# Performance work log

Measured on AMD Instinct MI355X. Metric: run time of the kernel, lower is better.

The kernel has to match this reference:

```python
import jax, jax.numpy as jnp
import numpy as np
from jax import lax

DIM = 256
NH = 16          # num_heads; head_dim = DIM//NH == NH (required by scale broadcast)
HD = DIM // NH   # 16
HID = int(DIM * 1.0)  # mlp hidden (ffn_expansion_factor=1.0)
B, H, W = 4, 128, 128
EPS = 1e-5


def _conv(x, w, pad, groups=1):
    # x: NCHW, w: OIHW
    return lax.conv_general_dilated(x, w, (1, 1), [(pad, pad), (pad, pad)],
                                    dimension_numbers=('NCHW', 'OIHW', 'NCHW'),
                                    feature_group_count=groups)


def _ln(x, w, b):
    # WithBias LayerNorm over channel axis (torch does it in b,(hw),c layout -> axis=c)
    mu = x.mean(1, keepdims=True)
    var = ((x - mu) ** 2).mean(1, keepdims=True)
    return (x - mu) / jnp.sqrt(var + EPS) * w[None, :, None, None] + b[None, :, None, None]


def setup_inputs() -> dict:
    key = jax.random.key(0)
    ks = jax.random.split(key, 12)
    s = 0.02
    return {
        'x': jax.random.normal(ks[0], (B, DIM, H, W), jnp.float32),
        'ln1_w': jnp.ones((DIM,), jnp.float32),
        'ln1_b': jnp.zeros((DIM,), jnp.float32),
        'conv3_w': jax.random.normal(ks[1], (DIM, 1, 3, 3), jnp.float32) * s,
        'conv3_b': jnp.zeros((DIM,), jnp.float32),
        'conv5_w': jax.random.normal(ks[2], (DIM, 1, 5, 5), jnp.float32) * s,
        'conv5_b': jnp.zeros((DIM,), jnp.float32),
        'qkv_w': jax.random.normal(ks[3], (3 * DIM, DIM), jnp.float32) * s,  # 1x1 conv, no bias
        'scale': jnp.ones((NH, 1, 1), jnp.float32),
        'g1_w': jax.random.normal(ks[4], (DIM // 4, DIM), jnp.float32) * s,
        'g1_b': jnp.zeros((DIM // 4,), jnp.float32),
        'g2_w': jax.random.normal(ks[5], (2, DIM // 4), jnp.float32) * s,
        'g2_b': jnp.zeros((2,), jnp.float32),
        'proj_w': jax.random.normal(ks[6], (DIM, DIM), jnp.float32) * s,
        'proj_b': jnp.zeros((DIM,), jnp.float32),
        'ln2_w': jnp.ones((DIM,), jnp.float32),
        'ln2_b': jnp.zeros((DIM,), jnp.float32),
        'pin_w': jax.random.normal(ks[7], (2 * HID, DIM), jnp.float32) * s,  # 1x1, bias=False
        'dw_w': jax.random.normal(ks[8], (2 * HID, 2, 3, 3), jnp.float32) * s,  # groups=HID
        'pout_w': jax.random.normal(ks[9], (DIM, HID), jnp.float32) * s,
    }


def _forward(x, ln1_w, ln1_b, conv3_w, conv3_b, conv5_w, conv5_b, qkv_w, scale,
             g1_w, g1_b, g2_w, g2_b, proj_w, proj_b, ln2_w, ln2_b, pin_w, dw_w, pout_w):
    b, c, h, w = x.shape
    # ---- token mixer (CAFormer) ----
    y = _ln(x, ln1_w, ln1_b)
    conv_feat = (_conv(y, conv3_w, 1, groups=DIM) + conv3_b[None, :, None, None]
                 + _conv(y, conv5_w, 2, groups=DIM) + conv5_b[None, :, None, None])
    qkv = jnp.einsum('oc,bchw->bohw', qkv_w, y)  # (b, 3c, h, w)
    q, k, v = jnp.split(qkv.reshape(b, 3, NH, HD, h * w), 3, axis=1)
    q, k, v = q[:, 0], k[:, 0], v[:, 0]  # (b, nh, hd, h*w)
    # L2 normalize over entire flattened spatial extent (F.normalize, eps=1e-12)
    q = q / jnp.maximum(jnp.linalg.norm(q, axis=-1, keepdims=True), 1e-12)
    k = k / jnp.maximum(jnp.linalg.norm(k, axis=-1, keepdims=True), 1e-12)
    q4 = q.reshape(b, NH, HD, h, w)
    k4 = k.reshape(b, NH, HD, h, w)
    v4 = v.reshape(b, NH, HD, h, w)
    # scale (nh,1,1) right-aligned against (b,nh,hd,x,x): broadcasts along hd axis
    sc = scale.reshape(1, 1, NH, 1, 1)
    # horizontal (row) attention: per (b,head,hd-channel), rows attend to rows
    attn_h = jax.nn.softmax(jnp.einsum('bhdxy,bhdzy->bhdxz', q4, k4) * sc, axis=-1)
    out_h = jnp.einsum('bhdxz,bhdzy->bhdxy', attn_h, v4).reshape(b, c, h, w)
    # vertical (column) attention
    qt, kt, vt = (t.swapaxes(-1, -2) for t in (q4, k4, v4))  # (b,nh,hd,w,h)
    attn_v = jax.nn.softmax(jnp.einsum('bhdyx,bhdzx->bhdyz', qt, kt) * sc, axis=-1)
    out_v = jnp.einsum('bhdyz,bhdzx->bhdyx', attn_v, vt).swapaxes(-1, -2).reshape(b, c, h, w)
    attn_feat = out_h + out_v
    # gate: GAP -> 1x1 -> relu -> 1x1 -> softmax over the 2 branch logits
    gp = y.mean((2, 3))  # (b, c)
    g = jax.nn.relu(gp @ g1_w.T + g1_b)
    g = jax.nn.softmax(g @ g2_w.T + g2_b, axis=-1)  # (b, 2)
    cw = g[:, 0][:, None, None, None]
    aw = g[:, 1][:, None, None, None]
    mixed = cw * conv_feat + aw * attn_feat
    tm = jnp.einsum('oc,bchw->bohw', proj_w, mixed) + proj_b[None, :, None, None]
    x = x + tm
    # ---- MLP ----
    y2 = _ln(x, ln2_w, ln2_b)
    p = jnp.einsum('oc,bchw->bohw', pin_w, y2)  # (b, 2*HID, h, w)
    dwo = _conv(p, dw_w, 1, groups=HID)         # grouped 3x3, 2 ch per group
    x1, x2 = dwo[:, :HID], dwo[:, HID:]
    m = jax.nn.gelu(x1, approximate=False) * x2
    mlp = jnp.einsum('oc,bchw->bohw', pout_w, m)
    return x + mlp


def reference(x, ln1_w, ln1_b, conv3_w, conv3_b, conv5_w, conv5_b, qkv_w, scale,
              g1_w, g1_b, g2_w, g2_b, proj_w, proj_b, ln2_w, ln2_b, pin_w, dw_w, pout_w):
    return _forward(x, ln1_w, ln1_b, conv3_w, conv3_b, conv5_w, conv5_b, qkv_w, scale,
                    g1_w, g1_b, g2_w, g2_b, proj_w, proj_b, ln2_w, ln2_b, pin_w, dw_w, pout_w)
```

## Files before the change

### kernel.cpp

```cpp
#include <hip/hip_runtime.h>
#include <hip/hip_bf16.h>
#include <math.h>

#define DIMC 256
#define NB   4
#define HH   128
#define WW   128
#define HWs  16384
#define HID  256
#define C2   512
#define EPSf 1e-5f

typedef __hip_bfloat16 bf;
typedef unsigned short u16;
typedef unsigned int   u32;
typedef float f32x4  __attribute__((ext_vector_type(4)));
typedef u32   u32x4  __attribute__((ext_vector_type(4)));
typedef short bf16x8 __attribute__((ext_vector_type(8)));

__device__ __forceinline__ float b2f(bf v){ return __bfloat162float(v); }
__device__ __forceinline__ bf    f2b(float v){ return __float2bfloat16(v); }
__device__ __forceinline__ float ldf(const float* p){ return *p; }
__device__ __forceinline__ float ldf(const bf* p){ return __bfloat162float(*p); }
__device__ __forceinline__ void  sto(float* p, float v){ *p = v; }
__device__ __forceinline__ void  sto(bf* p, float v){ *p = f2b(v); }
__device__ __forceinline__ void unpack2(u32 u, float& a, float& b){
  union{u32 x; float f;} lo, hi;
  lo.x = u << 16; hi.x = u & 0xffff0000u;
  a = lo.f; b = hi.f;
}
__device__ __forceinline__ u32 pack2(float a, float b){
  bf h0 = f2b(a), h1 = f2b(b);
  return (u32)*(u16*)&h0 | ((u32)*(u16*)&h1 << 16);
}
__device__ __forceinline__ void unp4(uint2 u, float* d){
  unpack2(u.x, d[0], d[1]); unpack2(u.y, d[2], d[3]);
}

__device__ __forceinline__ float gelu_exact(float v){
  return 0.5f*v*(1.0f + erff(v*0.70710678118654752f));
}

__global__ __launch_bounds__(256) void cvt_kernel(const float* __restrict__ s,
    u16* __restrict__ d, int n){
  int i = blockIdx.x*256 + threadIdx.x;
  if (i < n){ bf h = f2b(s[i]); d[i] = *(u16*)&h; }
}

template<typename TI>
__global__ __launch_bounds__(256) void ln_kernel(const TI* __restrict__ x,
    const float* __restrict__ w, const float* __restrict__ bb, bf* __restrict__ y){
  int p = blockIdx.x*256 + threadIdx.x;
  int b  = p >> 14;
  int sp = p & (HWs-1);
  const TI* xb = x + (size_t)b*DIMC*HWs + sp;
  float s = 0.f, s2 = 0.f;
  for(int c=0;c<DIMC;c++){ float v = ldf(xb + (size_t)c*HWs); s += v; s2 += v*v; }
  float mu   = s * (1.0f/DIMC);
  float var  = s2 * (1.0f/DIMC) - mu*mu;
  float rinv = rsqrtf(var + EPSf);
  bf* yb = y + (size_t)b*DIMC*HWs + sp;
  for(int c=0;c<DIMC;c++){
    float v = ldf(xb + (size_t)c*HWs);
    yb[(size_t)c*HWs] = f2b((v - mu)*rinv*w[c] + bb[c]);
  }
}

__global__ __launch_bounds__(256) void gp_kernel(const bf* __restrict__ y, float* __restrict__ gp){
  int bc = blockIdx.x;
  const bf* pl = y + (size_t)bc*HWs;
  float s = 0.f;
  for(int i=threadIdx.x;i<HWs;i+=256) s += b2f(pl[i]);
  __shared__ float red[256];
  red[threadIdx.x] = s; __syncthreads();
  for(int o=128;o>0;o>>=1){
    if(threadIdx.x<o) red[threadIdx.x] += red[threadIdx.x+o];
    __syncthreads();
  }
  if(threadIdx.x==0) gp[bc] = red[0]*(1.0f/HWs);
}

__global__ __launch_bounds__(256) void gate_kernel(const float* __restrict__ gp,
    const float* __restrict__ g1w, const float* __restrict__ g1b,
    const float* __restrict__ g2w, const float* __restrict__ g2b,
    float* __restrict__ cwaw){
  __shared__ float h[NB][64];
  __shared__ float zz[NB][2];
  int t = threadIdx.x;
  int b = t >> 6, j = t & 63;
  const float* gpb = gp + b*DIMC;
  const float* wr  = g1w + j*DIMC;
  float s = g1b[j];
  for(int c=0;c<DIMC;c++) s += gpb[c]*wr[c];
  h[b][j] = fmaxf(s, 0.f);
  __syncthreads();
  if (t < 8){
    int b2 = t >> 1, o = t & 1;
    float z = g2b[o];
    const float* w2 = g2w + o*64;
    for(int q=0;q<64;q++) z += w2[q]*h[b2][q];
    zz[b2][o] = z;
  }
  __syncthreads();
  if (t < 4){
    float z0 = zz[t][0], z1 = zz[t][1];
    float mm = fmaxf(z0,z1);
    float e0 = __expf(z0-mm), e1 = __expf(z1-mm);
    float inv = 1.0f/(e0+e1);
    cwaw[2*t]   = e0*inv;
    cwaw[2*t+1] = e1*inv;
  }
}

__global__ __launch_bounds__(256) void dwconv_kernel(const bf* __restrict__ y,
    const float* __restrict__ w3, const float* __restrict__ b3,
    const float* __restrict__ w5, const float* __restrict__ b5,
    bf* __restrict__ out){
  int bi = blockIdx.x;
  int strip = bi & 7;
  int c  = (bi >> 3) & 255;
  int b  = bi >> 11;
  int t = threadIdx.x;
  int sx = t & 15, ry = t >> 4;
  int hy = strip*16 + ry;
  int x0 = sx << 3;
  const u16* pl = (const u16*)y + ((size_t)(b*DIMC + c))*HWs;

  float kc[25];
  #pragma unroll
  for(int i=0;i<25;i++) kc[i] = w5[c*25+i];
  #pragma unroll
  for(int di=0;di<3;di++)
    #pragma unroll
    for(int dj=0;dj<3;dj++)
      kc[(di+1)*5 + (dj+1)] += w3[c*9 + di*3 + dj];
  float bia = b3[c] + b5[c];

  float acc[8];
  #pragma unroll
  for(int j=0;j<8;j++) acc[j] = bia;

  #pragma unroll
  for(int di=-2; di<=2; di++){
    int yy = hy + di;
    float row[16];
    if ((unsigned)yy < 128u){
      const u16* rp = pl + yy*WW;
      uint2 z; z.x = 0u; z.y = 0u;
      uint2 c0 = (x0 > 0)   ? *(const uint2*)(rp + x0 - 4) : z;
      uint2 c1 = *(const uint2*)(rp + x0);
      uint2 c2 = *(const uint2*)(rp + x0 + 4);
      uint2 c3 = (x0 < 120) ? *(const uint2*)(rp + x0 + 8) : z;
      unp4(c0, row); unp4(c1, row+4); unp4(c2, row+8); unp4(c3, row+12);
    } else {
      #pragma unroll
      for(int j=0;j<16;j++) row[j] = 0.f;
    }
    #pragma unroll
    for(int dj=-2; dj<=2; dj++){
      float w = kc[(di+2)*5 + (dj+2)];
      #pragma unroll
      for(int j=0;j<8;j++) acc[j] += row[4+j+dj]*w;
    }
  }
  u32x4 res;
  #pragma unroll
  for(int q=0;q<4;q++) ((u32*)&res)[q] = pack2(acc[2*q], acc[2*q+1]);
  *(u32x4*)((u16*)out + ((size_t)(b*DIMC + c))*HWs + hy*WW + x0) = res;
}

__global__ __launch_bounds__(256) void dwconv2_glu_kernel(const bf* __restrict__ p,
    const float* __restrict__ w, bf* __restrict__ m){
  int bi = blockIdx.x;
  int strip = bi & 7;
  int op = (bi >> 3) & 127;
  int b  = bi >> 10;
  int o0 = op*2, o1 = o0+1;
  int t = threadIdx.x;
  int sx = t & 15, ry = t >> 4;
  int hy = strip*16 + ry;
  int x0 = sx << 3;
  const u16* p0 = (const u16*)p + ((size_t)b*C2 + o0)*HWs;
  const u16* p1 = p0 + HWs;
  const u16* p2 = p0 + (size_t)256*HWs;
  const u16* p3 = p2 + HWs;

  float KA0[9], KA1[9], KA2[9], KA3[9];
  float KB0[9], KB1[9], KB2[9], KB3[9];
  #pragma unroll
  for(int i=0;i<9;i++){
    KA0[i] = w[o0*18 + i];        KA1[i] = w[o0*18 + 9 + i];
    KA2[i] = w[(o0+256)*18 + i];  KA3[i] = w[(o0+256)*18 + 9 + i];
    KB0[i] = w[o1*18 + i];        KB1[i] = w[o1*18 + 9 + i];
    KB2[i] = w[(o1+256)*18 + i];  KB3[i] = w[(o1+256)*18 + 9 + i];
  }

  float a1A[8] = {}, a2A[8] = {}, a1B[8] = {}, a2B[8] = {};
  #pragma unroll
  for(int di=-1; di<=1; di++){
    int yy = hy + di;
    if ((unsigned)yy >= 128u) continue;
    int roff = yy*WW;
    float r0[16], r1[16], r2[16], r3[16];
    uint2 z; z.x = 0u; z.y = 0u;
    bool lo = (x0 > 0), hi = (x0 < 120);
    {
      const u16* rp = p0 + roff;
      uint2 c0 = lo ? *(const uint2*)(rp + x0 - 4) : z;
      uint2 c1 = *(const uint2*)(rp + x0);
      uint2 c2 = *(const uint2*)(rp + x0 + 4);
      uint2 c3 = hi ? *(const uint2*)(rp + x0 + 8) : z;
      unp4(c0, r0); unp4(c1, r0+4); unp4(c2, r0+8); unp4(c3, r0+12);
    }
    {
      const u16* rp = p1 + roff;
      uint2 c0 = lo ? *(const uint2*)(rp + x0 - 4) : z;
      uint2 c1 = *(const uint2*)(rp + x0);
      uint2 c2 = *(const uint2*)(rp + x0 + 4);
      uint2 c3 = hi ? *(const uint2*)(rp + x0 + 8) : z;
      unp4(c0, r1); unp4(c1, r1+4); unp4(c2, r1+8); unp4(c3, r1+12);
    }
    {
      const u16* rp = p2 + roff;
      uint2 c0 = lo ? *(const uint2*)(rp + x0 - 4) : z;
      uint2 c1 = *(const uint2*)(rp + x0);
      uint2 c2 = *(const uint2*)(rp + x0 + 4);
      uint2 c3 = hi ? *(const uint2*)(rp + x0 + 8) : z;
      unp4(c0, r2); unp4(c1, r2+4); unp4(c2, r2+8); unp4(c3, r2+12);
    }
    {
      const u16* rp = p3 + roff;
      uint2 c0 = lo ? *(const uint2*)(rp + x0 - 4) : z;
      uint2 c1 = *(const uint2*)(rp + x0);
      uint2 c2 = *(const uint2*)(rp + x0 + 4);
      uint2 c3 = hi ? *(const uint2*)(rp + x0 + 8) : z;
      unp4(c0, r3); unp4(c1, r3+4); unp4(c2, r3+8); unp4(c3, r3+12);
    }
    #pragma unroll
    for(int dj=-1; dj<=1; dj++){
      int ki = (di+1)*3 + (dj+1);
      #pragma unroll
      for(int j=0;j<8;j++){
        int ii = 4+j+dj;
        a1A[j] += r0[ii]*KA0[ki] + r1[ii]*KA1[ki];
        a2A[j] += r2[ii]*KA2[ki] + r3[ii]*KA3[ki];
        a1B[j] += r0[ii]*KB0[ki] + r1[ii]*KB1[ki];
        a2B[j] += r2[ii]*KB2[ki] + r3[ii]*KB3[ki];
      }
    }
  }
  size_t obase = ((size_t)(b*DIMC + o0))*HWs + hy*WW + x0;
  u32x4 resA, resB;
  #pragma unroll
  for(int q=0;q<4;q++){
    ((u32*)&resA)[q] = pack2(gelu_exact(a1A[2*q])*a2A[2*q],
                             gelu_exact(a1A[2*q+1])*a2A[2*q+1]);
    ((u32*)&resB)[q] = pack2(gelu_exact(a1B[2*q])*a2B[2*q],
                             gelu_exact(a1B[2*q+1])*a2B[2*q+1]);
  }
  *(u32x4*)((u16*)m + obase) = resA;
  *(u32x4*)((u16*)m + obase + HWs) = resB;
}

template<typename TRES, typename TOUT>
__global__ __launch_bounds__(256, 2) void mfma_gemm(
    const u16* __restrict__ Wb, const bf* __restrict__ act,
    const float* __restrict__ bias, const TRES* __restrict__ resid,
    TOUT* __restrict__ out, int Oc)
{
  __shared__ u16 Bs[2][4096];
  int t  = threadIdx.x;
  int n0 = blockIdx.x * 128;
  int o0 = blockIdx.y * 128;
  int b  = n0 >> 14;
  int sp = n0 & (HWs-1);
  const u16* actu = (const u16*)act + (size_t)b*256*HWs + sp;

  int kp = t & 15;
  int ns = (t >> 4) << 3;
  int lane = t & 63;
  int wv = t >> 6;
  int wr = (wv >> 1) << 6;
  int wc = (wv & 1) << 6;
  int fr = lane & 15;
  int kg = lane >> 4;

  f32x4 acc[4][4] = {};

  auto stage = [&](int ks, int buf){
    const u16* r0 = actu + (size_t)(ks*32 + 2*kp)*HWs + ns;
    u32x4 u = *(const u32x4*)r0;
    u32x4 v = *(const u32x4*)(r0 + HWs);
    u32 w0=(u.x&0xffffu)|(v.x<<16), w1=(u.x>>16)|(v.x&0xffff0000u);
    u32 w2=(u.y&0xffffu)|(v.y<<16), w3=(u.y>>16)|(v.y&0xffff0000u);
    u32 w4=(u.z&0xffffu)|(v.z<<16), w5=(u.z>>16)|(v.z&0xffff0000u);
    u32 w6=(u.w&0xffffu)|(v.w<<16), w7=(u.w>>16)|(v.w&0xffff0000u);
    u16* bp = Bs[buf];
    int c0 = kp*2;
    *(u32*)&bp[(ns+0)*32+c0]=w0; *(u32*)&bp[(ns+1)*32+c0]=w1;
    *(u32*)&bp[(ns+2)*32+c0]=w2; *(u32*)&bp[(ns+3)*32+c0]=w3;
    *(u32*)&bp[(ns+4)*32+c0]=w4; *(u32*)&bp[(ns+5)*32+c0]=w5;
    *(u32*)&bp[(ns+6)*32+c0]=w6; *(u32*)&bp[(ns+7)*32+c0]=w7;
  };

  stage(0, 0);
  #pragma unroll
  for(int ks=0; ks<8; ++ks){
    int cur = ks & 1;
    __syncthreads();
    if (ks < 7) stage(ks+1, cur^1);
    bf16x8 af[4], bfr[4];
    #pragma unroll
    for(int i=0;i<4;i++)
      af[i] = *(const bf16x8*)(Wb + (size_t)(o0+wr+i*16+fr)*256 + ks*32 + kg*8);
    #pragma unroll
    for(int j=0;j<4;j++)
      bfr[j] = *(const bf16x8*)&Bs[cur][(wc + j*16 + fr)*32 + kg*8];
    #pragma unroll
    for(int i=0;i<4;i++)
      #pragma unroll
      for(int j=0;j<4;j++)
        acc[i][j] = __builtin_amdgcn_mfma_f32_16x16x32_bf16(af[i], bfr[j], acc[i][j], 0, 0, 0);
  }

  #pragma unroll
  for(int i=0;i<4;i++){
    #pragma unroll
    for(int reg=0;reg<4;reg++){
      int o = o0 + wr + i*16 + kg*4 + reg;
      size_t rowoff = ((size_t)b*Oc + o)*HWs + sp + wc + fr;
      float bia = bias ? bias[o] : 0.f;
      #pragma unroll
      for(int j=0;j<4;j++){
        float val = acc[i][j][reg] + bia;
        size_t pidx = rowoff + (size_t)(j*16);
        if (resid) val += ldf(resid + pidx);
        sto(out + pidx, val);
      }
    }
  }
}

__global__ __launch_bounds__(256) void norm_kernel(const bf* __restrict__ qkv,
    const float* __restrict__ scale, float* __restrict__ lscale){
  int s = blockIdx.x;
  int b = s >> 8, ch = s & 255;
  const bf* qp = qkv + ((size_t)b*768 + ch)*HWs;
  const bf* kp = qp + (size_t)256*HWs;
  float sq=0.f, sk=0.f;
  for(int i=threadIdx.x;i<HWs;i+=256){
    float a = b2f(qp[i]); sq += a*a;
    float c = b2f(kp[i]); sk += c*c;
  }
  __shared__ float r1[256], r2[256];
  r1[threadIdx.x]=sq; r2[threadIdx.x]=sk;
  __syncthreads();
  for(int o=128;o>0;o>>=1){
    if(threadIdx.x<o){ r1[threadIdx.x]+=r1[threadIdx.x+o]; r2[threadIdx.x]+=r2[threadIdx.x+o]; }
    __syncthreads();
  }
  if(threadIdx.x==0){
    float nq = fmaxf(sqrtf(r1[0]), 1e-12f);
    float nk = fmaxf(sqrtf(r2[0]), 1e-12f);
    lscale[s] = scale[ch & 15] / (nq*nk);
  }
}

#define SWB(r,c2) ((r)*256 + ((c2) ^ (((r)&7)<<4)))

__global__ __launch_bounds__(256, 2) void attn_mfma(const bf* __restrict__ qkv,
    const float* __restrict__ lscale, bf* __restrict__ outp,
    const bf* __restrict__ conv, const float* __restrict__ cwaw){
  __shared__ u16 LB0[16384];
  __shared__ u16 LB1[16384];
  int s  = blockIdx.x;
  int b  = s >> 8;
  int ch = s & 255;
  const u16* qp = (const u16*)qkv + ((size_t)b*768 + ch)*HWs;
  const u16* kp = qp + (size_t)256*HWs;
  const u16* vp = qp + (size_t)512*HWs;
  int t = threadIdx.x;
  float ls = lscale[s];

  int lane = t & 63, wvi = t >> 6;
  int fr = lane & 15, kg = lane >> 4;
  int nb = wvi << 5;
  int rr = t >> 1, hb = (t & 1) << 7;

  auto stage_nat = [&](const u16* src, u16* dst){
    #pragma unroll
    for(int i=0;i<8;i++){
      int c2 = hb + i*16;
      u32x4 v = *(const u32x4*)((const char*)src + rr*256 + c2);
      *(u32x4*)((char*)dst + SWB(rr, c2)) = v;
    }
  };
  auto stage_tr = [&](const u16* src, u16* dst){
    int kp2 = (t & 15)*2, cs = (t >> 4) << 3;
    #pragma unroll
    for(int base=0;base<128;base+=32){
      int sr = base + kp2;
      u32x4 u = *(const u32x4*)(src + sr*128 + cs);
      u32x4 v = *(const u32x4*)(src + (sr+1)*128 + cs);
      #pragma unroll
      for(int j=0;j<8;j++){
        u32 uw = ((const u32*)&u)[j>>1];
        u32 vw = ((const u32*)&v)[j>>1];
        u32 wv = (j&1) ? ((uw>>16) | (vw & 0xffff0000u))
                       : ((uw & 0xffffu) | (vw<<16));
        *(u32*)((char*)dst + SWB(cs+j, sr*2)) = wv;
      }
    }
  };

  f32x4 acc[8][2];
  f32x4 oacc[8][2];
  const f32x4 vzero = {};

  auto mmloop = [&](const u16* afsrc, const u16* bfsrc, f32x4 (&A)[8][2]){
    #pragma unroll
    for(int kk=0;kk<128;kk+=32){
      int kb2 = kk*2 + kg*16;
      bf16x8 b0 = *(const bf16x8*)((const char*)bfsrc + SWB(nb+fr,    kb2));
      bf16x8 b1 = *(const bf16x8*)((const char*)bfsrc + SWB(nb+16+fr, kb2));
      #pragma unroll
      for(int mt=0;mt<8;mt++){
        bf16x8 a0 = *(const bf16x8*)((const char*)afsrc + SWB(mt*16+fr, kb2));
        A[mt][0] = __builtin_amdgcn_mfma_f32_16x16x32_bf16(a0, b0, A[mt][0], 0, 0, 0);
        A[mt][1] = __builtin_amdgcn_mfma_f32_16x16x32_bf16(a0, b1, A[mt][1], 0, 0, 0);
      }
    }
  };

  auto writeCT = [&](u16* dst, f32x4 (&A)[8][2]){
    #pragma unroll
    for(int nt=0;nt<2;nt++){
      int n = nb + nt*16 + fr;
      #pragma unroll
      for(int mt=0;mt<8;mt++){
        #pragma unroll
        for(int pr=0;pr<2;pr++){
          u32 wv = pack2(A[mt][nt][pr*2], A[mt][nt][pr*2+1]);
          int z2 = (mt*16 + kg*4 + pr*2)*2;
          *(u32*)((char*)dst + SWB(n, z2)) = wv;
        }
      }
    }
  };

  auto softmax = [&](){
    #pragma unroll
    for(int nt=0;nt<2;nt++){
      float mx = -1e30f;
      #pragma unroll
      for(int mt=0;mt<8;mt++)
        #pragma unroll
        for(int rg=0;rg<4;rg++){
          acc[mt][nt][rg] *= ls;
          mx = fmaxf(mx, acc[mt][nt][rg]);
        }
      mx = fmaxf(mx, __shfl_xor(mx,16));
      mx = fmaxf(mx, __shfl_xor(mx,32));
      float sm = 0.f;
      #pragma unroll
      for(int mt=0;mt<8;mt++)
        #pragma unroll
        for(int rg=0;rg<4;rg++){
          float e = __expf(acc[mt][nt][rg]-mx);
          acc[mt][nt][rg] = e; sm += e;
        }
      sm += __shfl_xor(sm,16);
      sm += __shfl_xor(sm,32);
      float inv = 1.0f/sm;
      #pragma unroll
      for(int mt=0;mt<8;mt++)
        #pragma unroll
        for(int rg=0;rg<4;rg++)
          acc[mt][nt][rg] *= inv;
    }
  };

  stage_nat(kp, LB0); stage_nat(qp, LB1);
  __syncthreads();
  #pragma unroll
  for(int mt=0;mt<8;mt++){ acc[mt][0]=vzero; acc[mt][1]=vzero; }
  mmloop(LB0, LB1, acc);
  softmax();
  __syncthreads();
  writeCT(LB0, acc);
  stage_tr(vp, LB1);
  __syncthreads();
  #pragma unroll
  for(int mt=0;mt<8;mt++){ oacc[mt][0]=vzero; oacc[mt][1]=vzero; }
  mmloop(LB1, LB0, oacc);
  __syncthreads();

  stage_tr(kp, LB0); stage_tr(qp, LB1);
  __syncthreads();
  #pragma unroll
  for(int mt=0;mt<8;mt++){ acc[mt][0]=vzero; acc[mt][1]=vzero; }
  mmloop(LB0, LB1, acc);
  softmax();
  __syncthreads();
  writeCT(LB0, acc);
  stage_nat(vp, LB1);
  __syncthreads();
  mmloop(LB0, LB1, oacc);
  __syncthreads();

  writeCT(LB0, oacc);
  __syncthreads();

  float cw = cwaw[2*b], aw = cwaw[2*b+1];
  const u16* cp = (const u16*)conv + ((size_t)b*DIMC + ch)*HWs;
  bf* op = outp + ((size_t)b*DIMC + ch)*HWs;
  #pragma unroll
  for(int i=0;i<8;i++){
    int c2 = hb + i*16;
    u32x4 ov = *(const u32x4*)((char*)LB0 + SWB(rr, c2));
    u32x4 cv = *(const u32x4*)(cp + rr*128 + c2/2);
    u32x4 res;
    #pragma unroll
    for(int q=0;q<4;q++){
      float o0,o1,c0,c1;
      unpack2(((u32*)&ov)[q], o0, o1);
      unpack2(((u32*)&cv)[q], c0, c1);
      ((u32*)&res)[q] = pack2(cw*c0 + aw*o0, cw*c1 + aw*o1);
    }
    *(u32x4*)((u16*)op + rr*128 + c2/2) = res;
  }
}

extern "C" void kernel_launch(void* const* d_in, const int* in_sizes, int n_in,
                              void* d_out, int out_size, void* d_ws, size_t ws_size,
                              hipStream_t stream){
  (void)in_sizes; (void)n_in; (void)out_size; (void)ws_size;
  const float* x       = (const float*)d_in[0];
  const float* ln1_w   = (const float*)d_in[1];
  const float* ln1_b   = (const float*)d_in[2];
  const float* conv3_w = (const float*)d_in[3];
  const float* conv3_b = (const float*)d_in[4];
  const float* conv5_w = (const float*)d_in[5];
  const float* conv5_b = (const float*)d_in[6];
  const float* qkv_w   = (const float*)d_in[7];
  const float* scale   = (const float*)d_in[8];
  const float* g1_w    = (const float*)d_in[9];
  const float* g1_b    = (const float*)d_in[10];
  const float* g2_w    = (const float*)d_in[11];
  const float* g2_b    = (const float*)d_in[12];
  const float* proj_w  = (const float*)d_in[13];
  const float* proj_b  = (const float*)d_in[14];
  const float* ln2_w   = (const float*)d_in[15];
  const float* ln2_b   = (const float*)d_in[16];
  const float* pin_w   = (const float*)d_in[17];
  const float* dw_w    = (const float*)d_in[18];
  const float* pout_w  = (const float*)d_in[19];
  float* out = (float*)d_out;
  char* wsb  = (char*)d_ws;

  const size_t MB = 1024*1024;
  bf* y    = (bf*)(wsb +   0*MB);
  bf* conv = (bf*)(wsb +  32*MB);
  bf* qkv  = (bf*)(wsb +  64*MB);
  bf* attnf= (bf*)(wsb +   0*MB);
  bf* xnew = (bf*)(wsb +  64*MB);
  bf* y2   = (bf*)(wsb +  96*MB);
  bf* p    = (bf*)(wsb +   0*MB);
  bf* m    = (bf*)(wsb +  96*MB);
  u16* Wqkv  = (u16*)(wsb + 160*MB);
  u16* Wproj = Wqkv + 196608;
  u16* Wpin  = Wproj + 65536;
  u16* Wpout = Wpin + 131072;
  float* gp     = (float*)(Wpout + 65536);
  float* cwaw   = gp + 1024;
  float* lscale = cwaw + 16;

  cvt_kernel<<<768,256,0,stream>>>(qkv_w,  Wqkv, 196608);
  cvt_kernel<<<256,256,0,stream>>>(proj_w, Wproj, 65536);
  cvt_kernel<<<512,256,0,stream>>>(pin_w,  Wpin, 131072);
  cvt_kernel<<<256,256,0,stream>>>(pout_w, Wpout, 65536);

  ln_kernel<float><<<256,256,0,stream>>>(x, ln1_w, ln1_b, y);
  gp_kernel<<<1024,256,0,stream>>>(y, gp);
  gate_kernel<<<1,256,0,stream>>>(gp, g1_w, g1_b, g2_w, g2_b, cwaw);
  dwconv_kernel<<<8192,256,0,stream>>>(y, conv3_w, conv3_b, conv5_w, conv5_b, conv);
  mfma_gemm<float,bf><<<dim3(512,6),256,0,stream>>>(Wqkv, y, nullptr,
                                        (const float*)nullptr, qkv, 768);
  norm_kernel<<<1024,256,0,stream>>>(qkv, scale, lscale);
  attn_mfma<<<1024,256,0,stream>>>(qkv, lscale, attnf, conv, cwaw);
  mfma_gemm<float,bf><<<dim3(512,2),256,0,stream>>>(Wproj, attnf, proj_b, x, xnew, 256);
  ln_kernel<bf><<<256,256,0,stream>>>(xnew, ln2_w, ln2_b, y2);
  mfma_gemm<float,bf><<<dim3(512,4),256,0,stream>>>(Wpin, y2, nullptr,
                                        (const float*)nullptr, p, 512);
  dwconv2_glu_kernel<<<4096,256,0,stream>>>(p, dw_w, m);
  mfma_gemm<bf,float><<<dim3(512,2),256,0,stream>>>(Wpout, m, nullptr, xnew, out, 256);
}
```

Measured before the change: 484.4 us.

## Fuse q/k norm reduction into attention kernel and software-pipeline GEMM loads

Removes the separate norm_kernel by computing the sum of squares of q and k while they are staged into shared memory in the attention kernel, reducing via wave shuffles and a small shared array. This avoids a full extra read of q and k and one kernel launch. Separately, the MFMA GEMM now issues the next K-slice's global loads (activations and weights) before the MFMAs and writes to LDS afterwards, so load latency overlaps with compute. The cost is higher register pressure from the prefetched values.

```diff
diff --git a/kernel.cpp b/kernel.cpp
--- a/kernel.cpp
+++ b/kernel.cpp
@@ -287,10 +287,12 @@
 
   f32x4 acc[4][4] = {};
 
-  auto stage = [&](int ks, int buf){
+  auto stage_load = [&](int ks, u32x4& u, u32x4& v){
     const u16* r0 = actu + (size_t)(ks*32 + 2*kp)*HWs + ns;
-    u32x4 u = *(const u32x4*)r0;
-    u32x4 v = *(const u32x4*)(r0 + HWs);
+    u = *(const u32x4*)r0;
+    v = *(const u32x4*)(r0 + HWs);
+  };
+  auto stage_write = [&](const u32x4& u, const u32x4& v, int buf){
     u32 w0=(u.x&0xffffu)|(v.x<<16), w1=(u.x>>16)|(v.x&0xffff0000u);
     u32 w2=(u.y&0xffffu)|(v.y<<16), w3=(u.y>>16)|(v.y&0xffff0000u);
     u32 w4=(u.z&0xffffu)|(v.z<<16), w5=(u.z>>16)|(v.z&0xffff0000u);
@@ -302,17 +304,29 @@
     *(u32*)&bp[(ns+4)*32+c0]=w4; *(u32*)&bp[(ns+5)*32+c0]=w5;
     *(u32*)&bp[(ns+6)*32+c0]=w6; *(u32*)&bp[(ns+7)*32+c0]=w7;
   };
-
-  stage(0, 0);
+  auto loadA = [&](int ks, bf16x8* af){
+    #pragma unroll
+    for(int i=0;i<4;i++)
+      af[i] = *(const bf16x8*)(Wb + (size_t)(o0+wr+i*16+fr)*256 + ks*32 + kg*8);
+  };
+
+  bf16x8 afc[4], afn[4];
+  loadA(0, afc);
+  {
+    u32x4 u, v;
+    stage_load(0, u, v);
+    stage_write(u, v, 0);
+  }
   #pragma unroll
   for(int ks=0; ks<8; ++ks){
     int cur = ks & 1;
     __syncthreads();
-    if (ks < 7) stage(ks+1, cur^1);
-    bf16x8 af[4], bfr[4];
-    #pragma unroll
-    for(int i=0;i<4;i++)
-      af[i] = *(const bf16x8*)(Wb + (size_t)(o0+wr+i*16+fr)*256 + ks*32 + kg*8);
+    u32x4 su, sv;
+    if (ks < 7){
+      stage_load(ks+1, su, sv);
+      loadA(ks+1, afn);
+    }
+    bf16x8 bfr[4];
     #pragma unroll
     for(int j=0;j<4;j++)
       bfr[j] = *(const bf16x8*)&Bs[cur][(wc + j*16 + fr)*32 + kg*8];
@@ -320,7 +334,12 @@
     for(int i=0;i<4;i++)
       #pragma unroll
       for(int j=0;j<4;j++)
-        acc[i][j] = __builtin_amdgcn_mfma_f32_16x16x32_bf16(af[i], bfr[j], acc[i][j], 0, 0, 0);
+        acc[i][j] = __builtin_amdgcn_mfma_f32_16x16x32_bf16(afc[i], bfr[j], acc[i][j], 0, 0, 0);
+    if (ks < 7){
+      stage_write(su, sv, cur^1);
+      #pragma unroll
+      for(int i=0;i<4;i++) afc[i] = afn[i];
+    }
   }
 
   #pragma unroll
@@ -341,38 +360,14 @@
   }
 }
 
-__global__ __launch_bounds__(256) void norm_kernel(const bf* __restrict__ qkv,
-    const float* __restrict__ scale, float* __restrict__ lscale){
-  int s = blockIdx.x;
-  int b = s >> 8, ch = s & 255;
-  const bf* qp = qkv + ((size_t)b*768 + ch)*HWs;
-  const bf* kp = qp + (size_t)256*HWs;
-  float sq=0.f, sk=0.f;
-  for(int i=threadIdx.x;i<HWs;i+=256){
-    float a = b2f(qp[i]); sq += a*a;
-    float c = b2f(kp[i]); sk += c*c;
-  }
-  __shared__ float r1[256], r2[256];
-  r1[threadIdx.x]=sq; r2[threadIdx.x]=sk;
-  __syncthreads();
-  for(int o=128;o>0;o>>=1){
-    if(threadIdx.x<o){ r1[threadIdx.x]+=r1[threadIdx.x+o]; r2[threadIdx.x]+=r2[threadIdx.x+o]; }
-    __syncthreads();
-  }
-  if(threadIdx.x==0){
-    float nq = fmaxf(sqrtf(r1[0]), 1e-12f);
-    float nk = fmaxf(sqrtf(r2[0]), 1e-12f);
-    lscale[s] = scale[ch & 15] / (nq*nk);
-  }
-}
-
 #define SWB(r,c2) ((r)*256 + ((c2) ^ (((r)&7)<<4)))
 
 __global__ __launch_bounds__(256, 2) void attn_mfma(const bf* __restrict__ qkv,
-    const float* __restrict__ lscale, bf* __restrict__ outp,
+    const float* __restrict__ scale, bf* __restrict__ outp,
     const bf* __restrict__ conv, const float* __restrict__ cwaw){
   __shared__ u16 LB0[16384];
   __shared__ u16 LB1[16384];
+  __shared__ float2 red2[4];
   int s  = blockIdx.x;
   int b  = s >> 8;
   int ch = s & 255;
@@ -380,7 +375,6 @@
   const u16* kp = qp + (size_t)256*HWs;
   const u16* vp = qp + (size_t)512*HWs;
   int t = threadIdx.x;
-  float ls = lscale[s];
 
   int lane = t & 63, wvi = t >> 6;
   int fr = lane & 15, kg = lane >> 4;
@@ -394,6 +388,22 @@
       u32x4 v = *(const u32x4*)((const char*)src + rr*256 + c2);
       *(u32x4*)((char*)dst + SWB(rr, c2)) = v;
     }
+  };
+  auto stage_nat_sum = [&](const u16* src, u16* dst) -> float {
+    float ssum = 0.f;
+    #pragma unroll
+    for(int i=0;i<8;i++){
+      int c2 = hb + i*16;
+      u32x4 v = *(const u32x4*)((const char*)src + rr*256 + c2);
+      *(u32x4*)((char*)dst + SWB(rr, c2)) = v;
+      #pragma unroll
+      for(int q=0;q<4;q++){
+        float a0, a1;
+        unpack2(((u32*)&v)[q], a0, a1);
+        ssum += a0*a0 + a1*a1;
+      }
+    }
+    return ssum;
   };
   auto stage_tr = [&](const u16* src, u16* dst){
     int kp2 = (t & 15)*2, cs = (t >> 4) << 3;
@@ -416,6 +426,7 @@
   f32x4 acc[8][2];
   f32x4 oacc[8][2];
   const f32x4 vzero = {};
+  float ls = 0.f;
 
   auto mmloop = [&](const u16* afsrc, const u16* bfsrc, f32x4 (&A)[8][2]){
     #pragma unroll
@@ -480,8 +491,23 @@
     }
   };
 
-  stage_nat(kp, LB0); stage_nat(qp, LB1);
-  __syncthreads();
+  float sk = stage_nat_sum(kp, LB0);
+  float sq = stage_nat_sum(qp, LB1);
+  #pragma unroll
+  for(int off=1; off<64; off<<=1){
+    sq += __shfl_xor(sq, off);
+    sk += __shfl_xor(sk, off);
+  }
+  if (lane == 0) red2[wvi] = make_float2(sq, sk);
+  __syncthreads();
+  {
+    float tq = 0.f, tk = 0.f;
+    #pragma unroll
+    for(int wI=0;wI<4;wI++){ tq += red2[wI].x; tk += red2[wI].y; }
+    float nq = fmaxf(sqrtf(tq), 1e-12f);
+    float nk = fmaxf(sqrtf(tk), 1e-12f);
+    ls = scale[ch & 15] / (nq*nk);
+  }
   #pragma unroll
   for(int mt=0;mt<8;mt++){ acc[mt][0]=vzero; acc[mt][1]=vzero; }
   mmloop(LB0, LB1, acc);
@@ -573,7 +599,6 @@
   u16* Wpout = Wpin + 131072;
   float* gp     = (float*)(Wpout + 65536);
   float* cwaw   = gp + 1024;
-  float* lscale = cwaw + 16;
 
   cvt_kernel<<<768,256,0,stream>>>(qkv_w,  Wqkv, 196608);
   cvt_kernel<<<256,256,0,stream>>>(proj_w, Wproj, 65536);
@@ -586,8 +611,7 @@
   dwconv_kernel<<<8192,256,0,stream>>>(y, conv3_w, conv3_b, conv5_w, conv5_b, conv);
   mfma_gemm<float,bf><<<dim3(512,6),256,0,stream>>>(Wqkv, y, nullptr,
                                         (const float*)nullptr, qkv, 768);
-  norm_kernel<<<1024,256,0,stream>>>(qkv, scale, lscale);
-  attn_mfma<<<1024,256,0,stream>>>(qkv, lscale, attnf, conv, cwaw);
+  attn_mfma<<<1024,256,0,stream>>>(qkv, scale, attnf, conv, cwaw);
   mfma_gemm<float,bf><<<dim3(512,2),256,0,stream>>>(Wproj, attnf, proj_b, x, xnew, 256);
   ln_kernel<bf><<<256,256,0,stream>>>(xnew, ln2_w, ln2_b, y2);
   mfma_gemm<float,bf><<<dim3(512,4),256,0,stream>>>(Wpin, y2, nullptr,
```

After: 520.9 us. 7.5% more time.
